# Performance work log

Hardware: AMD Instinct MI355X
Metric: run time of the kernel (lower is better)

Reference implementation:

```python
import jax, jax.numpy as jnp
import numpy as np

B, S, D = 2, 2048, 2048
H, KVH = 32, 8
HD = D // H            # 64
G = H // KVH           # 4 query heads per kv head
CLIP = 8.0
THETA = 500000.0
EPS = 1e-6
SCALE = 1.0 / np.sqrt(HD)


def setup_inputs() -> dict:
    key = jax.random.key(0)
    ks = jax.random.split(key, 4)
    hidden_states = jax.random.normal(ks[0], (B, S, D), dtype=jnp.float32)
    attention_mask = jnp.ones((B, S), dtype=jnp.int32)
    position_ids = jnp.broadcast_to(jnp.arange(S, dtype=jnp.int32)[None, :], (B, S))
    causal_mask = jnp.tril(jnp.ones((S, S), dtype=bool))[None, None]
    std = 0.02
    w_qkv = jax.random.normal(ks[1], (D, D + 2 * KVH * HD), dtype=jnp.float32) * std
    w_out = jax.random.normal(ks[2], (D, D), dtype=jnp.float32) * std
    ln1_scale = jnp.ones((D,), dtype=jnp.float32)
    ln2_scale = jnp.ones((D,), dtype=jnp.float32)
    return {
        "hidden_states": hidden_states,
        "attention_mask": attention_mask,
        "position_ids": position_ids,
        "causal_mask": causal_mask,
        "ln1_scale": ln1_scale,
        "w_qkv": w_qkv,
        "w_out": w_out,
        "ln2_scale": ln2_scale,
    }


def _layernorm(x, scale):
    m = jnp.mean(x, axis=-1, keepdims=True)
    v = jnp.mean(jnp.square(x - m), axis=-1, keepdims=True)
    return (x - m) * jax.lax.rsqrt(v + EPS) * scale


def _rope(x, cos, sin):
    # neox style: rotate halves of head_dim. x: [B,S,h,HD], cos/sin: [B,S,1,HD/2]
    x1, x2 = jnp.split(x, 2, axis=-1)
    return jnp.concatenate([x1 * cos - x2 * sin, x2 * cos + x1 * sin], axis=-1)


def _forward(hidden_states, attention_mask, position_ids, causal_mask,
             ln1_scale, w_qkv, w_out, ln2_scale):
    residual = hidden_states
    x = _layernorm(hidden_states, ln1_scale)

    qkv = jnp.clip(x @ w_qkv, -CLIP, CLIP)  # [B,S,D+2*KVH*HD]
    q, kv = jnp.split(qkv, [D], axis=2)
    k, v = jnp.split(kv, [KVH * HD], axis=2)
    q = q.reshape(B, S, H, HD)
    k = k.reshape(B, S, KVH, HD)
    v = v.reshape(B, S, KVH, HD)

    inv_freq = 1.0 / (THETA ** (jnp.arange(0, HD, 2, dtype=jnp.float32) / HD))
    ang = position_ids.astype(jnp.float32)[..., None] * inv_freq  # [B,S,HD/2]
    cos = jnp.cos(ang)[:, :, None, :]
    sin = jnp.sin(ang)[:, :, None, :]
    q = _rope(q, cos, sin)
    k = _rope(k, cos, sin)

    # GQA: group query heads per kv head
    qg = q.reshape(B, S, KVH, G, HD)
    scores = jnp.einsum("bqhgd,bkhd->bhgqk", qg, k) * SCALE  # [B,KVH,G,S,S]
    mask = causal_mask[:, :, :S, :S] & (attention_mask[:, None, None, :] > 0)  # [B,1,S,S]
    bias = jnp.where(mask[:, :, None], 0.0, jnp.finfo(scores.dtype).min)
    probs = jax.nn.softmax(scores + bias, axis=-1)
    attn = jnp.einsum("bhgqk,bkhd->bqhgd", probs, v).reshape(B, S, D)

    attn_out = attn @ w_out
    hidden = attn_out + residual
    residual2 = hidden
    hidden = _layernorm(hidden, ln2_scale)
    return residual2, hidden


def reference(hidden_states, attention_mask, position_ids, causal_mask,
              ln1_scale, w_qkv, w_out, ln2_scale):
    return _forward(hidden_states, attention_mask, position_ids, causal_mask,
                    ln1_scale, w_qkv, w_out, ln2_scale)
```

## Files before the change

### kernel.cpp

```cpp
#include <hip/hip_runtime.h>
#include <hip/hip_bf16.h>
#include <stdint.h>

typedef __bf16 bf16_t;
typedef __bf16 bf16x8 __attribute__((ext_vector_type(8)));
typedef float f32x4 __attribute__((ext_vector_type(4)));
typedef _Float16 f16x8v __attribute__((ext_vector_type(8)));
typedef _Float16 f16x4v __attribute__((ext_vector_type(4)));

#define LOG2E 1.44269504088896f

__device__ __forceinline__ void load_lds16(const void* g, void* l) {
  __builtin_amdgcn_global_load_lds(
      (__attribute__((address_space(1))) unsigned int*)(uintptr_t)(g),
      (__attribute__((address_space(3))) unsigned int*)(l),
      16, 0, 0);
}

__device__ __forceinline__ f16x4v pack4_f16(float a, float b, float c, float d) {
  const __fp16 __attribute__((ext_vector_type(2))) lo = __builtin_amdgcn_cvt_pkrtz(a, b);
  const __fp16 __attribute__((ext_vector_type(2))) hi = __builtin_amdgcn_cvt_pkrtz(c, d);
  return __builtin_bit_cast(f16x4v, __builtin_shufflevector(lo, hi, 0, 1, 2, 3));
}

__global__ __launch_bounds__(256) void ln_kernel(
    const float* __restrict__ in, const float* __restrict__ gamma,
    bf16_t* __restrict__ out_bf, float* __restrict__ out_f)
{
  const int row = blockIdx.x;
  const int t = threadIdx.x;
  const float* x = in + (size_t)row * 2048;
  float4 a = ((const float4*)x)[t];
  float4 b = ((const float4*)x)[t + 256];
  float v[8] = {a.x, a.y, a.z, a.w, b.x, b.y, b.z, b.w};
  float s = 0.f, q = 0.f;
#pragma unroll
  for (int i = 0; i < 8; ++i) { s += v[i]; q += v[i] * v[i]; }
#pragma unroll
  for (int off = 1; off < 64; off <<= 1) {
    s += __shfl_xor(s, off, 64);
    q += __shfl_xor(q, off, 64);
  }
  __shared__ float red[4][2];
  if ((t & 63) == 0) { red[t >> 6][0] = s; red[t >> 6][1] = q; }
  __syncthreads();
  s = red[0][0] + red[1][0] + red[2][0] + red[3][0];
  q = red[0][1] + red[1][1] + red[2][1] + red[3][1];
  const float mean = s * (1.0f / 2048.0f);
  const float var = q * (1.0f / 2048.0f) - mean * mean;
  const float inv = rsqrtf(var + 1e-6f);
  float4 ga = ((const float4*)gamma)[t];
  float4 gb = ((const float4*)gamma)[t + 256];
  float g[8] = {ga.x, ga.y, ga.z, ga.w, gb.x, gb.y, gb.z, gb.w};
  float y[8];
#pragma unroll
  for (int i = 0; i < 8; ++i) y[i] = (v[i] - mean) * inv * g[i];
  if (out_bf) {
    alignas(16) bf16_t tb[8];
#pragma unroll
    for (int i = 0; i < 8; ++i) tb[i] = (bf16_t)y[i];
    bf16_t* o = out_bf + (size_t)row * 2048;
    *(uint2*)(o + t * 4) = *(const uint2*)(tb);
    *(uint2*)(o + (t + 256) * 4) = *(const uint2*)(tb + 4);
  } else {
    float* o = out_f + (size_t)row * 2048;
    ((float4*)o)[t] = make_float4(y[0], y[1], y[2], y[3]);
    ((float4*)o)[t + 256] = make_float4(y[4], y[5], y[6], y[7]);
  }
}

__global__ __launch_bounds__(256) void fused_pre(
    const float* __restrict__ hid, const float* __restrict__ ln1g,
    bf16_t* __restrict__ xb,
    const float* __restrict__ wqkv, const float* __restrict__ wout,
    bf16_t* __restrict__ wT, bf16_t* __restrict__ wOT,
    float2* __restrict__ tbl)
{
  const int bid = blockIdx.x;
  const int t = threadIdx.x;
  if (bid < 4096) {
    const float* x = hid + (size_t)bid * 2048;
    float4 a = ((const float4*)x)[t];
    float4 b = ((const float4*)x)[t + 256];
    float v[8] = {a.x, a.y, a.z, a.w, b.x, b.y, b.z, b.w};
    float s = 0.f, q = 0.f;
#pragma unroll
    for (int i = 0; i < 8; ++i) { s += v[i]; q += v[i] * v[i]; }
#pragma unroll
    for (int off = 1; off < 64; off <<= 1) {
      s += __shfl_xor(s, off, 64);
      q += __shfl_xor(q, off, 64);
    }
    __shared__ float red[4][2];
    if ((t & 63) == 0) { red[t >> 6][0] = s; red[t >> 6][1] = q; }
    __syncthreads();
    s = red[0][0] + red[1][0] + red[2][0] + red[3][0];
    q = red[0][1] + red[1][1] + red[2][1] + red[3][1];
    const float mean = s * (1.0f / 2048.0f);
    const float var = q * (1.0f / 2048.0f) - mean * mean;
    const float inv = rsqrtf(var + 1e-6f);
    float4 ga = ((const float4*)ln1g)[t];
    float4 gb = ((const float4*)ln1g)[t + 256];
    float g[8] = {ga.x, ga.y, ga.z, ga.w, gb.x, gb.y, gb.z, gb.w};
    alignas(16) bf16_t tb[8];
#pragma unroll
    for (int i = 0; i < 8; ++i) tb[i] = (bf16_t)((v[i] - mean) * inv * g[i]);
    bf16_t* o = xb + (size_t)bid * 2048;
    *(uint2*)(o + t * 4) = *(const uint2*)(tb);
    *(uint2*)(o + (t + 256) * 4) = *(const uint2*)(tb + 4);
    return;
  }
  if (bid >= 14336) {
    const int idx = (bid - 14336) * 256 + t;
    const int p = idx >> 5, i = idx & 31;
    const float inv = exp2f(-0.59161151f * (float)i);
    float sn, cs;
    sincosf((float)p * inv, &sn, &cs);
    tbl[idx] = make_float2(cs, sn);
    return;
  }
  const bool isQ = bid < 10240;
  const int i6 = isQ ? (bid - 4096) : (bid - 10240);
  const int bx = isQ ? (i6 % 96) : (i6 & 63);
  const int by = isQ ? (i6 / 96) : (i6 >> 6);
  const float* in = isQ ? wqkv : wout;
  bf16_t* out = isQ ? wT : wOT;
  const int in_stride = isQ ? 3072 : 2048;
  const int c0 = bx * 32, r0 = by * 32;
  __shared__ float tile[32][33];
  const int r = t >> 3, c4 = (t & 7) * 4;
  const float4 v4 = *(const float4*)(in + (size_t)(r0 + r) * in_stride + c0 + c4);
  tile[r][c4] = v4.x; tile[r][c4 + 1] = v4.y;
  tile[r][c4 + 2] = v4.z; tile[r][c4 + 3] = v4.w;
  __syncthreads();
  const int cc = t >> 3, rr4 = (t & 7) * 4;
  alignas(8) bf16_t obuf[4];
#pragma unroll
  for (int j = 0; j < 4; ++j) obuf[j] = (bf16_t)tile[rr4 + j][cc];
  *(uint2*)(out + (size_t)(c0 + cc) * 2048 + r0 + rr4) = *(const uint2*)obuf;
}

__global__ __launch_bounds__(256) void kv_prep(
    const _Float16* __restrict__ qkv, const int* __restrict__ pos_ids,
    const float2* __restrict__ tbl,
    _Float16* __restrict__ ko, _Float16* __restrict__ vt)
{
  const int bid = blockIdx.x;
  const int t = threadIdx.x;
  if (bid < 512) {
    const int lr = t >> 5, u = t & 31;
    const int bs = bid * 8 + lr;
    const int b = bs >> 11, s = bs & 2047;
    const int hh = u >> 2, i8 = (u & 3) * 8;
    const _Float16* row = qkv + (size_t)bs * 3072 + 2048 + hh * 64;
    const float2* tp = tbl + (size_t)pos_ids[bs] * 32 + i8;
    const f16x8v x1v = *(const f16x8v*)(row + i8);
    const f16x8v x2v = *(const f16x8v*)(row + 32 + i8);
    f16x8v y1, y2;
#pragma unroll
    for (int j = 0; j < 8; ++j) {
      const float2 cs = tp[j];
      const float x1 = (float)x1v[j], x2 = (float)x2v[j];
      y1[j] = (_Float16)(x1 * cs.x - x2 * cs.y);
      y2[j] = (_Float16)(x2 * cs.x + x1 * cs.y);
    }
    _Float16* d = ko + (((size_t)b * 8 + hh) * 2048 + s) * 64 + i8;
    *(f16x8v*)(d) = y1;
    *(f16x8v*)(d + 32) = y2;
    return;
  }
  const int idx = bid - 512;
  const int bz = idx >> 10;
  const int rem = idx & 1023;
  const int bx = rem & 15, by = rem >> 4;
  const _Float16* ib = qkv + (size_t)bz * 2048 * 3072 + 2560;
  _Float16* ob = vt + (size_t)bz * 512 * 2048;
  const int c0 = bx * 32, r0 = by * 32;
  __shared__ float tile[32][33];
  const int r = t >> 3, c4 = (t & 7) * 4;
  const f16x4v v4 = *(const f16x4v*)(ib + (size_t)(r0 + r) * 3072 + c0 + c4);
#pragma unroll
  for (int j = 0; j < 4; ++j) tile[r][c4 + j] = (float)v4[j];
  __syncthreads();
  const int cc = t >> 3, rr4 = (t & 7) * 4;
  alignas(8) _Float16 obuf[4];
#pragma unroll
  for (int j = 0; j < 4; ++j) obuf[j] = (_Float16)tile[rr4 + j][cc];
  *(uint2*)(ob + (size_t)(c0 + cc) * 2048 + r0 + rr4) = *(const uint2*)obuf;
}

__global__ __launch_bounds__(256) void gemm_bt(
    const bf16_t* __restrict__ A, const bf16_t* __restrict__ BT,
    int M, int N, int K, int mode,
    const float* __restrict__ resid, void* __restrict__ outv)
{
  __shared__ alignas(16) bf16_t As[128 * 32];
  __shared__ alignas(16) bf16_t Bs[128 * 32];
  const int t = threadIdx.x;
  const int lane = t & 63;
  const int wave = t >> 6;
  const int m0 = blockIdx.y * 128;
  const int n0 = blockIdx.x * 128;
  const int wm = (wave >> 1) * 64;
  const int wn = (wave & 1) * 64;

  f32x4 acc[4][4] = {};

  const int i0 = t, i1 = t + 256;
  const bf16_t* Ag0 = A + (size_t)(m0 + (i0 >> 2)) * K + (i0 & 3) * 8;
  const bf16_t* Ag1 = A + (size_t)(m0 + (i1 >> 2)) * K + (i1 & 3) * 8;
  const bf16_t* Bg0 = BT + (size_t)(n0 + (i0 >> 2)) * K + (i0 & 3) * 8;
  const bf16_t* Bg1 = BT + (size_t)(n0 + (i1 >> 2)) * K + (i1 & 3) * 8;
  bf16_t* AsW0 = As + (size_t)(wave * 64) * 8;
  bf16_t* AsW1 = As + (size_t)(256 + wave * 64) * 8;
  bf16_t* BsW0 = Bs + (size_t)(wave * 64) * 8;
  bf16_t* BsW1 = Bs + (size_t)(256 + wave * 64) * 8;

  const int rsel = lane & 15;
  const int ksel = (lane >> 4) * 8;

  for (int k0 = 0; k0 < K; k0 += 32) {
    __syncthreads();
    load_lds16(Ag0 + k0, AsW0);
    load_lds16(Ag1 + k0, AsW1);
    load_lds16(Bg0 + k0, BsW0);
    load_lds16(Bg1 + k0, BsW1);
    __syncthreads();
    bf16x8 af[4], bfr[4];
#pragma unroll
    for (int i = 0; i < 4; ++i) {
      af[i]  = *(const bf16x8*)(As + (wm + i * 16 + rsel) * 32 + ksel);
      bfr[i] = *(const bf16x8*)(Bs + (wn + i * 16 + rsel) * 32 + ksel);
    }
#pragma unroll
    for (int mi = 0; mi < 4; ++mi)
#pragma unroll
      for (int ni = 0; ni < 4; ++ni)
        acc[mi][ni] = __builtin_amdgcn_mfma_f32_16x16x32_bf16(af[mi], bfr[ni], acc[mi][ni], 0, 0, 0);
  }

  const int row_l = (lane >> 4) * 4;
  const int col_l = lane & 15;
#pragma unroll
  for (int mi = 0; mi < 4; ++mi) {
#pragma unroll
    for (int ni = 0; ni < 4; ++ni) {
      const size_t base = (size_t)(m0 + wm + mi * 16 + row_l) * N + (size_t)(n0 + wn + ni * 16 + col_l);
#pragma unroll
      for (int r = 0; r < 4; ++r) {
        float vv = acc[mi][ni][r];
        if (mode == 0) {
          vv = fminf(8.0f, fmaxf(-8.0f, vv));
          ((_Float16*)outv)[base + (size_t)r * N] = (_Float16)vv;
        } else {
          ((float*)outv)[base + (size_t)r * N] = vv + resid[base + (size_t)r * N];
        }
      }
    }
  }
}

#define STAGE_TO(J, SI) do { \
    _Float16* d_ = &KV[(SI)][ksel][wv4]; \
    const _Float16* s_ = gsrc + (size_t)(J) * gstep; \
    load_lds16(s_, d_); \
    load_lds16(s_ + 32, d_ + 2048); \
  } while (0)

#define ABODY(J, BI, SI) do { \
    const int j_ = (J); \
    if (j_ == nit - 1) asm volatile("s_waitcnt vmcnt(0)" ::: "memory"); \
    else               asm volatile("s_waitcnt vmcnt(2)" ::: "memory"); \
    __builtin_amdgcn_s_barrier(); \
    __builtin_amdgcn_sched_barrier(0); \
    if (j_ + 2 < nit) STAGE_TO(j_ + 2, SI); \
    const _Float16* Kbuf = &KV[(BI)][0][0]; \
    const _Float16* Vbuf = &KV[(BI)][1][0]; \
    f32x4 st[4] = {}; \
    __builtin_amdgcn_s_setprio(1); \
    _Pragma("unroll") \
    for (int mt_ = 0; mt_ < 4; ++mt_) { \
      const f16x8v kf0_ = *(const f16x8v*)(Kbuf + krowc[mt_]); \
      const f16x8v kf1_ = *(const f16x8v*)(Kbuf + 2048 + krowc[mt_]); \
      st[mt_] = __builtin_amdgcn_mfma_f32_16x16x32_f16(kf0_, qf0, st[mt_], 0, 0, 0); \
      st[mt_] = __builtin_amdgcn_mfma_f32_16x16x32_f16(kf1_, qf1, st[mt_], 0, 0, 0); \
    } \
    __builtin_amdgcn_s_setprio(0); \
     \
    f16x4v vA_[4], vB_[4], vC_[4], vD_[4]; \
    _Pragma("unroll") \
    for (int nt_ = 0; nt_ < 4; ++nt_) { \
      const _Float16* Vr_ = Vbuf + vrow[nt_]; \
      vA_[nt_] = *(const f16x4v*)(Vr_ + vca); \
      vB_[nt_] = *(const f16x4v*)(Vr_ + vcb); \
      vC_[nt_] = *(const f16x4v*)(Vr_ + 2048 + vca); \
      vD_[nt_] = *(const f16x4v*)(Vr_ + 2048 + vcb); \
    } \
    const int k0_ = j_ * 64; \
    if (k0_ + 64 > q0) { \
      _Pragma("unroll") \
      for (int mt_ = 0; mt_ < 4; ++mt_) \
        _Pragma("unroll") \
        for (int r_ = 0; r_ < 4; ++r_) { \
          if (k0_ + mt_ * 16 + lg * 4 + r_ > myq) st[mt_][r_] = -3.0e38f; \
        } \
    } \
     \
    const float x0_ = fmaxf(fmaxf(st[0][0], st[0][1]), st[0][2]); \
    const float x1_ = fmaxf(fmaxf(st[0][3], st[1][0]), st[1][1]); \
    const float x2_ = fmaxf(fmaxf(st[1][2], st[1][3]), st[2][0]); \
    const float x3_ = fmaxf(fmaxf(st[2][1], st[2][2]), st[2][3]); \
    const float x4_ = fmaxf(fmaxf(st[3][0], st[3][1]), st[3][2]); \
    float mx_ = fmaxf(fmaxf(fmaxf(x0_, x1_), fmaxf(x2_, x3_)), fmaxf(x4_, st[3][3])); \
    if (__any(mx_ > m_r + 8.0f)) {   \
      mx_ = fmaxf(mx_, __shfl_xor(mx_, 16, 64)); \
      mx_ = fmaxf(mx_, __shfl_xor(mx_, 32, 64)); \
      const float mn_ = fmaxf(m_r, mx_); \
      const float al_ = exp2f(m_r - mn_); \
      _Pragma("unroll") \
      for (int r_ = 0; r_ < 4; ++r_) { \
        const float ao_ = __shfl(al_, lg * 4 + r_, 16); \
        ov[0][r_] *= ao_; ov[1][r_] *= ao_; ov[2][r_] *= ao_; ov[3][r_] *= ao_; \
        ovl[r_] *= ao_; \
      } \
      m_r = mn_; \
    } \
    f16x4v pf_[4]; \
    _Pragma("unroll") \
    for (int mt_ = 0; mt_ < 4; ++mt_) { \
      pf_[mt_] = pack4_f16(exp2f(st[mt_][0] - m_r), exp2f(st[mt_][1] - m_r), \
                           exp2f(st[mt_][2] - m_r), exp2f(st[mt_][3] - m_r)); \
    } \
    __builtin_amdgcn_s_setprio(1); \
    _Pragma("unroll") \
    for (int nt_ = 0; nt_ < 4; ++nt_) { \
      ov[nt_] = __builtin_amdgcn_mfma_f32_16x16x16f16(pf_[0], vA_[nt_], ov[nt_], 0, 0, 0); \
      ov[nt_] = __builtin_amdgcn_mfma_f32_16x16x16f16(pf_[1], vB_[nt_], ov[nt_], 0, 0, 0); \
      ov[nt_] = __builtin_amdgcn_mfma_f32_16x16x16f16(pf_[2], vC_[nt_], ov[nt_], 0, 0, 0); \
      ov[nt_] = __builtin_amdgcn_mfma_f32_16x16x16f16(pf_[3], vD_[nt_], ov[nt_], 0, 0, 0); \
    } \
    ovl = __builtin_amdgcn_mfma_f32_16x16x16f16(pf_[0], onesv, ovl, 0, 0, 0); \
    ovl = __builtin_amdgcn_mfma_f32_16x16x16f16(pf_[1], onesv, ovl, 0, 0, 0); \
    ovl = __builtin_amdgcn_mfma_f32_16x16x16f16(pf_[2], onesv, ovl, 0, 0, 0); \
    ovl = __builtin_amdgcn_mfma_f32_16x16x16f16(pf_[3], onesv, ovl, 0, 0, 0); \
    __builtin_amdgcn_s_setprio(0); \
  } while (0)

__global__ __launch_bounds__(512, 4) void attn_kernel(
    const _Float16* __restrict__ qkv, const int* __restrict__ pos,
    const float2* __restrict__ tbl,
    const _Float16* __restrict__ Kb, const _Float16* __restrict__ Vt,
    bf16_t* __restrict__ Out)
{
  __shared__ alignas(16) _Float16 KV[3][2][4096];

  const int kvh = blockIdx.y;
  const int b = blockIdx.z;
  const int t = threadIdx.x;
  const int lane = t & 63;
  const int wave = t >> 6;
  const int g = wave >> 1;
  const int tile = wave & 1;
  const int h = kvh * 4 + g;
  const int ln15 = lane & 15;
  const int lg = lane >> 4;

  const _Float16* Kh = Kb + ((size_t)(b * 8 + kvh) * 2048) * 64;
  const _Float16* Vh = Vt + ((size_t)(b * 8 + kvh) * 64) * 2048;

  const bool stK = (t < 256);
  const int u = t & 255;
  const int srow = u >> 2;
  const int scol = ((u & 3) ^ ((srow >> 1) & 3)) * 8;
  const _Float16* gsrc = stK ? (Kh + (size_t)srow * 64 + scol)
                             : (Vh + (size_t)srow * 2048 + scol);
  const int gstep = stK ? 64 * 64 : 64;
  const int ksel = stK ? 0 : 1;
  const int wv4 = (wave & 3) * 512;

  const int svz = (ln15 >> 1) & 3;
  const int kc = (lg ^ svz) * 8;
  const int vca = ((lg >> 1) ^ svz) * 8 + (lg & 1) * 4;
  const int vcb = (((lg >> 1) + 2) ^ svz) * 8 + (lg & 1) * 4;
  int krowc[4], vrow[4];
#pragma unroll
  for (int i = 0; i < 4; ++i) {
    krowc[i] = (i * 16 + ln15) * 32 + kc;
    vrow[i] = (i * 16 + ln15) * 32;
  }
  const f16x4v onesv = {(_Float16)1.0f, (_Float16)1.0f, (_Float16)1.0f, (_Float16)1.0f};
  const float qsc = 0.125f * LOG2E;

  for (int half = 0; half < 2; ++half) {
    const int qc = (half == 0) ? blockIdx.x : (63 - blockIdx.x);
    const int q0 = qc * 32 + tile * 16;
    const int myq = q0 + ln15;
    const int nit = (qc >> 1) + 1;

    const _Float16* qrow = qkv + (size_t)(b * 2048 + myq) * 3072 + h * 64;
    const float2* tq = tbl + (size_t)pos[b * 2048 + myq] * 32 + lg * 8;
    const f16x8v qr0 = *(const f16x8v*)(qrow + lg * 8);
    const f16x8v qr1 = *(const f16x8v*)(qrow + 32 + lg * 8);
    f16x8v qf0, qf1;
#pragma unroll
    for (int j = 0; j < 8; ++j) {
      const float2 cs = tq[j];
      const float x1 = (float)qr0[j], x2 = (float)qr1[j];
      qf0[j] = (_Float16)((x1 * cs.x - x2 * cs.y) * qsc);
      qf1[j] = (_Float16)((x2 * cs.x + x1 * cs.y) * qsc);
    }

    f32x4 ov[4] = {};
    f32x4 ovl = {};
    float m_r = 0.0f;

    STAGE_TO(0, 0);
    if (nit > 1) STAGE_TO(1, 1);

    int it = 0;
    for (; it + 3 <= nit; it += 3) {
      ABODY(it, 0, 2);
      ABODY(it + 1, 1, 0);
      ABODY(it + 2, 2, 1);
    }
    if (it < nit) { ABODY(it, 0, 2); ++it; }
    if (it < nit) { ABODY(it, 1, 0); }

#pragma unroll
    for (int r = 0; r < 4; ++r) {
      const float ilo = 1.0f / ovl[r];
      const size_t obase = ((size_t)b * 2048 + (size_t)(q0 + lg * 4 + r)) * 2048 + (size_t)h * 64;
#pragma unroll
      for (int nt = 0; nt < 4; ++nt)
        Out[obase + nt * 16 + ln15] = (bf16_t)(ov[nt][r] * ilo);
    }
    __builtin_amdgcn_s_barrier();
    __builtin_amdgcn_sched_barrier(0);
  }
}
#undef ABODY
#undef STAGE_TO

extern "C" void kernel_launch(void* const* d_in, const int* in_sizes, int n_in,
                              void* d_out, int out_size, void* d_ws, size_t ws_size,
                              hipStream_t stream) {
  (void)in_sizes; (void)n_in; (void)out_size; (void)ws_size;
  const float* hid  = (const float*)d_in[0];
  const int*   pos  = (const int*)d_in[2];
  const float* ln1g = (const float*)d_in[4];
  const float* wqkv = (const float*)d_in[5];
  const float* wout = (const float*)d_in[6];
  const float* ln2g = (const float*)d_in[7];
  float* out = (float*)d_out;
  char* ws = (char*)d_ws;

  bf16_t*   xb  = (bf16_t*)(ws + 0);
  bf16_t*   wT  = (bf16_t*)(ws + 16777216);
  _Float16* qkv = (_Float16*)(ws + 29360128);
  float2*   tbl = (float2*)(ws + 54525952);
  bf16_t*   wOT = (bf16_t*)(ws + 55050240);
  _Float16* kb  = (_Float16*)(ws + 79691776);
  _Float16* vt  = (_Float16*)(ws + 83886080);

  fused_pre<<<14592, 256, 0, stream>>>(hid, ln1g, xb, wqkv, wout, wT, wOT, tbl);
  gemm_bt<<<dim3(24, 32), 256, 0, stream>>>(xb, wT, 4096, 3072, 2048, 0, nullptr, qkv);
  kv_prep<<<2560, 256, 0, stream>>>(qkv, pos, tbl, kb, vt);
  attn_kernel<<<dim3(32, 8, 2), 512, 0, stream>>>(qkv, pos, tbl, kb, vt, xb);
  gemm_bt<<<dim3(16, 32), 256, 0, stream>>>(xb, wOT, 4096, 2048, 2048, 1, hid, out);
  ln_kernel<<<4096, 256, 0, stream>>>(out, ln2g, nullptr, out + 8388608);
}
```

Measured before the change: 358.6 us.

## Triple-buffer GEMM LDS staging and swizzle workgroup order for L2 reuse

Replaces the single-buffered GEMM main loop, which had two barriers per k-step, with a three-stage LDS ring. Global-to-LDS loads are issued two iterations ahead and gated by vmcnt waits with a single barrier per step, so memory latency overlaps with MFMA work. It also remaps workgroup indices with a modulo-8 swizzle to improve cache locality, and raises wave priority around the MFMA block. In exchange, LDS use triples, which may reduce occupancy, and the swizzle assumes the workgroup count divides evenly by 8.

```diff
diff --git a/kernel.cpp b/kernel.cpp
--- a/kernel.cpp
+++ b/kernel.cpp
@@ -189,18 +189,52 @@
   *(uint2*)(ob + (size_t)(c0 + cc) * 2048 + r0 + rr4) = *(const uint2*)obuf;
 }
 
+#define GSTAGE(J, SI) do { \
+    const int kk_ = (J) * 32; \
+    load_lds16(Ag0 + kk_, As[SI] + w0off); \
+    load_lds16(Ag1 + kk_, As[SI] + w1off); \
+    load_lds16(Bg0 + kk_, Bs[SI] + w0off); \
+    load_lds16(Bg1 + kk_, Bs[SI] + w1off); \
+  } while (0)
+
+#define GBODY(J, BI, SI) do { \
+    if ((J) == nit - 1) asm volatile("s_waitcnt vmcnt(0)" ::: "memory"); \
+    else                asm volatile("s_waitcnt vmcnt(4)" ::: "memory"); \
+    __builtin_amdgcn_s_barrier(); \
+    __builtin_amdgcn_sched_barrier(0); \
+    if ((J) + 2 < nit) GSTAGE((J) + 2, SI); \
+    bf16x8 af_[4], bf_[4]; \
+    _Pragma("unroll") \
+    for (int i_ = 0; i_ < 4; ++i_) { \
+      af_[i_] = *(const bf16x8*)(As[BI] + (wm + i_ * 16 + rsel) * 32 + ksel); \
+      bf_[i_] = *(const bf16x8*)(Bs[BI] + (wn + i_ * 16 + rsel) * 32 + ksel); \
+    } \
+    __builtin_amdgcn_s_setprio(1); \
+    _Pragma("unroll") \
+    for (int mi_ = 0; mi_ < 4; ++mi_) \
+      _Pragma("unroll") \
+      for (int ni_ = 0; ni_ < 4; ++ni_) \
+        acc[mi_][ni_] = __builtin_amdgcn_mfma_f32_16x16x32_bf16(af_[mi_], bf_[ni_], acc[mi_][ni_], 0, 0, 0); \
+    __builtin_amdgcn_s_setprio(0); \
+  } while (0)
+
 __global__ __launch_bounds__(256) void gemm_bt(
     const bf16_t* __restrict__ A, const bf16_t* __restrict__ BT,
     int M, int N, int K, int mode,
     const float* __restrict__ resid, void* __restrict__ outv)
 {
-  __shared__ alignas(16) bf16_t As[128 * 32];
-  __shared__ alignas(16) bf16_t Bs[128 * 32];
+  __shared__ alignas(16) bf16_t As[3][128 * 32];
+  __shared__ alignas(16) bf16_t Bs[3][128 * 32];
   const int t = threadIdx.x;
   const int lane = t & 63;
   const int wave = t >> 6;
-  const int m0 = blockIdx.y * 128;
-  const int n0 = blockIdx.x * 128;
+
+  const int nwg = gridDim.x * gridDim.y;
+  const int flat = blockIdx.y * gridDim.x + blockIdx.x;
+  const int swz = (flat & 7) * (nwg >> 3) + (flat >> 3);
+  const int m0 = (swz / gridDim.x) * 128;
+  const int n0 = (swz % gridDim.x) * 128;
+
   const int wm = (wave >> 1) * 64;
   const int wn = (wave & 1) * 64;
 
@@ -211,33 +245,23 @@
   const bf16_t* Ag1 = A + (size_t)(m0 + (i1 >> 2)) * K + (i1 & 3) * 8;
   const bf16_t* Bg0 = BT + (size_t)(n0 + (i0 >> 2)) * K + (i0 & 3) * 8;
   const bf16_t* Bg1 = BT + (size_t)(n0 + (i1 >> 2)) * K + (i1 & 3) * 8;
-  bf16_t* AsW0 = As + (size_t)(wave * 64) * 8;
-  bf16_t* AsW1 = As + (size_t)(256 + wave * 64) * 8;
-  bf16_t* BsW0 = Bs + (size_t)(wave * 64) * 8;
-  bf16_t* BsW1 = Bs + (size_t)(256 + wave * 64) * 8;
+  const int w0off = (wave * 64) * 8;
+  const int w1off = (256 + wave * 64) * 8;
 
   const int rsel = lane & 15;
   const int ksel = (lane >> 4) * 8;
 
-  for (int k0 = 0; k0 < K; k0 += 32) {
-    __syncthreads();
-    load_lds16(Ag0 + k0, AsW0);
-    load_lds16(Ag1 + k0, AsW1);
-    load_lds16(Bg0 + k0, BsW0);
-    load_lds16(Bg1 + k0, BsW1);
-    __syncthreads();
-    bf16x8 af[4], bfr[4];
-#pragma unroll
-    for (int i = 0; i < 4; ++i) {
-      af[i]  = *(const bf16x8*)(As + (wm + i * 16 + rsel) * 32 + ksel);
-      bfr[i] = *(const bf16x8*)(Bs + (wn + i * 16 + rsel) * 32 + ksel);
-    }
-#pragma unroll
-    for (int mi = 0; mi < 4; ++mi)
-#pragma unroll
-      for (int ni = 0; ni < 4; ++ni)
-        acc[mi][ni] = __builtin_amdgcn_mfma_f32_16x16x32_bf16(af[mi], bfr[ni], acc[mi][ni], 0, 0, 0);
-  }
+  const int nit = K >> 5;
+  GSTAGE(0, 0);
+  GSTAGE(1, 1);
+  int it = 0;
+  for (; it + 3 <= nit; it += 3) {
+    GBODY(it, 0, 2);
+    GBODY(it + 1, 1, 0);
+    GBODY(it + 2, 2, 1);
+  }
+  if (it < nit) { GBODY(it, 0, 2); ++it; }
+  if (it < nit) { GBODY(it, 1, 0); }
 
   const int row_l = (lane >> 4) * 4;
   const int col_l = lane & 15;
@@ -259,6 +283,8 @@
     }
   }
 }
+#undef GBODY
+#undef GSTAGE
 
 #define STAGE_TO(J, SI) do { \
     _Float16* d_ = &KV[(SI)][ksel][wv4]; \
```

After: 381.4 us. +6.4%, slower.
